# Optimization experiments

Measured on AMD Instinct MI355X. Metric: run time of the kernel, lower is better.

## Reference

```python
import jax, jax.numpy as jnp
import numpy as np

RADIUS = 50.0
EPS = 1e-8


def setup_inputs() -> dict:
    key = jax.random.key(0)
    k1, k2, k3, k4, k5 = jax.random.split(key, 5)
    N, E, H = 16384, 524288, 256
    x = jax.random.normal(k1, (N, H), dtype=jnp.float32)
    edge_index = jax.random.randint(k2, (2, E), 0, N, dtype=jnp.int32)
    spatial_coords = jax.random.uniform(k3, (N, 2), dtype=jnp.float32) * 1000.0
    w1 = jax.random.normal(k4, (3, H // 2), dtype=jnp.float32) * 0.02
    b1 = jnp.zeros((H // 2,), dtype=jnp.float32)
    w2 = jax.random.normal(k5, (H // 2, H), dtype=jnp.float32) * 0.02
    b2 = jnp.zeros((H,), dtype=jnp.float32)
    return {"x": x, "edge_index": edge_index, "spatial_coords": spatial_coords,
            "w1": w1, "b1": b1, "w2": w2, "b2": b2}


def reference(x, edge_index, spatial_coords, w1, b1, w2, b2):
    N = x.shape[0]
    row, col = edge_index[0], edge_index[1]

    # degree via scatter-add (segment_sum)
    ones = jnp.ones(row.shape, dtype=x.dtype)
    degree = jax.ops.segment_sum(ones, row, num_segments=N)  # [N]

    # spatial density: count neighbors within RADIUS (full pairwise, vectorized)
    sq = jnp.sum(spatial_coords * spatial_coords, axis=-1)  # [N]
    d2 = sq[:, None] + sq[None, :] - 2.0 * (spatial_coords @ spatial_coords.T)  # [N,N] squared dists
    in_radius = (d2 <= RADIUS * RADIUS).astype(x.dtype)
    density = jnp.sum(in_radius, axis=1) - 1.0  # exclude self
    density = density / (jnp.max(density) + EPS)

    # local feature variance: || x - mean(neighbor features) ||
    nbr_sum = jax.ops.segment_sum(x[col], row, num_segments=N)  # [N,H]
    cnt = jnp.clip(degree, 1.0)[:, None]
    nbr_mean = nbr_sum / cnt
    fvar = jnp.linalg.norm(x - nbr_mean, axis=-1)  # [N]
    fvar = fvar / (jnp.max(fvar) + EPS)

    feats = jnp.stack([degree / (jnp.max(degree) + EPS), density, fvar], axis=-1)  # [N,3]
    h = jax.nn.relu(feats @ w1 + b1)
    return h @ w2 + b2  # [N, hidden_dim]
```

## Files before the change

kernel.cpp:

```cpp
#include <hip/hip_runtime.h>
#include <math.h>

#define R2 2500.0f
#define EPSF 1e-8f

constexpr int H   = 256;
constexpr int HH  = 128;
constexpr int NB  = 8;
constexpr int BSH = 11;
constexpr int RPW = 4;

__global__ void __launch_bounds__(256) k_degcell(
    const int* __restrict__ row, const int* __restrict__ col,
    int* __restrict__ deg4, const float* __restrict__ coords,
    int* __restrict__ cellcnt, int E, int EB, int N) {
    if ((int)blockIdx.x < EB) {
        int e = blockIdx.x * 256 + threadIdx.x;
        if (e < E) atomicAdd(&deg4[row[e] * NB + (col[e] >> BSH)], 1);
    } else {
        int t = ((int)blockIdx.x - EB) * 256 + threadIdx.x;
        if (t < N) {
            float2 c = ((const float2*)coords)[t];
            int cx = (int)(c.x * 0.02f); if (cx > 19) cx = 19;
            int cy = (int)(c.y * 0.02f); if (cy > 19) cy = 19;
            atomicAdd(&cellcnt[cy * 20 + cx], 1);
        }
    }
}

__global__ void __launch_bounds__(256) k_bsum(const int* __restrict__ deg4,
                                              int* __restrict__ bsum) {
    int t = threadIdx.x;
    int4 v = ((const int4*)deg4)[blockIdx.x * 256 + t];
    int sum = v.x + v.y + v.z + v.w;
#pragma unroll
    for (int off = 32; off > 0; off >>= 1) sum += __shfl_xor(sum, off, 64);
    __shared__ int sw[4];
    if ((t & 63) == 0) sw[t >> 6] = sum;
    __syncthreads();
    if (t == 0) bsum[blockIdx.x] = sw[0] + sw[1] + sw[2] + sw[3];
}

__global__ void __launch_bounds__(512) k_scatcell(
    const int* __restrict__ deg4, const int* __restrict__ bsum,
    int* __restrict__ rp4, int* __restrict__ cur4, int M,
    const int* __restrict__ cellcnt, int* __restrict__ cellstart,
    int* __restrict__ cellcur) {
    __shared__ int s[512];
    int t = threadIdx.x;
    int blk = blockIdx.x;
    if (blk < gridDim.x - 1) {
        s[t] = (t < 128) ? bsum[t] : 0;
        __syncthreads();
        for (int off = 1; off < 128; off <<= 1) {
            int v = (t < 128) ? s[t] : 0;
            int add = (t >= off && t < 128) ? s[t - off] : 0;
            __syncthreads();
            if (t < 128) s[t] = v + add;
            __syncthreads();
        }
        int boff = (blk > 0) ? s[blk - 1] : 0;
        if (t < 256) {
            int lane = t & 63, w = t >> 6;
            int4 v = ((const int4*)deg4)[blk * 256 + t];
            int tsum = v.x + v.y + v.z + v.w;
            int incl = tsum;
#pragma unroll
            for (int off = 1; off < 64; off <<= 1) {
                int n = __shfl_up(incl, off, 64);
                if (lane >= off) incl += n;
            }
            __shared__ int wsum[4];
            if (lane == 63) wsum[w] = incl;
            __syncthreads();
            int woff = 0;
#pragma unroll
            for (int k = 0; k < 4; k++) woff += (k < w) ? wsum[k] : 0;
            int excl = boff + woff + (incl - tsum);
            int4 r;
            r.x = excl;
            r.y = excl + v.x;
            r.z = excl + v.x + v.y;
            r.w = excl + v.x + v.y + v.z;
            ((int4*)rp4)[blk * 256 + t]  = r;
            ((int4*)cur4)[blk * 256 + t] = r;
            if (blk == 127 && t == 255) rp4[M] = excl + tsum;
        }
    } else {
        s[t] = (t < 400) ? cellcnt[t] : 0;
        __syncthreads();
        for (int off = 1; off < 512; off <<= 1) {
            int v = s[t];
            int add = (t >= off) ? s[t - off] : 0;
            __syncthreads();
            s[t] = v + add;
            __syncthreads();
        }
        if (t < 400) {
            int excl = (t > 0) ? s[t - 1] : 0;
            cellstart[t] = excl;
            cellcur[t]   = excl;
        }
        if (t == 400) cellstart[400] = s[399];
    }
}

__global__ void __launch_bounds__(256) k_fillcell(
    const int* __restrict__ row, const int* __restrict__ col,
    int* __restrict__ cur4, int* __restrict__ cols,
    const float* __restrict__ coords, int* __restrict__ cellcur,
    float4* __restrict__ pts, int E, int EB, int N) {
    if ((int)blockIdx.x < EB) {
        int e = blockIdx.x * 256 + threadIdx.x;
        if (e < E) {
            int r = row[e], c = col[e];
            int p = atomicAdd(&cur4[r * NB + (c >> BSH)], 1);
            cols[p] = c;
        }
    } else {
        int t = ((int)blockIdx.x - EB) * 256 + threadIdx.x;
        if (t < N) {
            float2 c = ((const float2*)coords)[t];
            int cx = (int)(c.x * 0.02f); if (cx > 19) cx = 19;
            int cy = (int)(c.y * 0.02f); if (cy > 19) cy = 19;
            int p = atomicAdd(&cellcur[cy * 20 + cx], 1);
            pts[p] = make_float4(c.x, c.y, c.x * c.x + c.y * c.y, __int_as_float(t));
        }
    }
}

__global__ void __launch_bounds__(256) k_dgrid(
    const float4* __restrict__ pts, const int* __restrict__ cellstart,
    int* __restrict__ dens, int N) {
    int wave = threadIdx.x >> 6;
    int lane = threadIdx.x & 63;
    int t = blockIdx.x * 4 + wave;
    float4 p = pts[t];
    int cx = (int)(p.x * 0.02f); if (cx > 19) cx = 19;
    int cy = (int)(p.y * 0.02f); if (cy > 19) cy = 19;
    int x0 = cx - 2; if (x0 < 0) x0 = 0;
    int x1 = cx + 2; if (x1 > 19) x1 = 19;
    int y0 = cy - 2; if (y0 < 0) y0 = 0;
    int y1 = cy + 2; if (y1 > 19) y1 = 19;
    int cnt = 0;
    for (int yy = y0; yy <= y1; yy++) {
        int rowb = yy * 20;
        int s = cellstart[rowb + x0];
        int e = cellstart[rowb + x1 + 1];
        for (int q = s + lane; q < e; q += 64) {
            float4 pq = pts[q];
            float dot = p.x * pq.x + p.y * pq.y;
            float d2 = (p.z + pq.z) - 2.0f * dot;
            cnt += (d2 <= R2) ? 1 : 0;
        }
    }
#pragma unroll
    for (int off = 32; off > 0; off >>= 1) cnt += __shfl_xor(cnt, off, 64);
    if (lane == 0) dens[__float_as_int(p.w)] = cnt;
}

__global__ void __launch_bounds__(256) k_fvar(
    const float* __restrict__ x, const int* __restrict__ rp4,
    const int* __restrict__ cols, float* __restrict__ fvar, int N) {
    __shared__ float4 lds[4][8][64];
    int wave = threadIdx.x >> 6;
    int lane = threadIdx.x & 63;
    int i0 = (blockIdx.x * 4 + wave) * RPW;
    const float4* xb = (const float4*)x;

    int bnd = rp4[i0 * NB + (lane < 32 ? lane : 32)];

    float4 acc0 = make_float4(0.f, 0.f, 0.f, 0.f);
    float4 acc1 = make_float4(0.f, 0.f, 0.f, 0.f);
    float4 acc2 = make_float4(0.f, 0.f, 0.f, 0.f);
    float4 acc3 = make_float4(0.f, 0.f, 0.f, 0.f);

    for (int b = 0; b < NB; b++) {
        int s0 = __shfl(bnd, b, 64),      e0 = __shfl(bnd, b + 1, 64);
        int s1 = __shfl(bnd, 8 + b, 64),  e1 = __shfl(bnd, 9 + b, 64);
        int s2 = __shfl(bnd, 16 + b, 64), e2 = __shfl(bnd, 17 + b, 64);
        int s3 = __shfl(bnd, 24 + b, 64), e3 = __shfl(bnd, 25 + b, 64);
        int m0 = e0 - s0, m1 = e1 - s1, m2 = e2 - s2;
        int c1 = m0, c2 = m0 + m1, c3 = m0 + m1 + m2;
        int mt = c3 + (e3 - s3);
        if (mt == 0) continue;

        int j = lane;
        int rowj = (j >= c1) + (j >= c2) + (j >= c3);
        int base = (rowj == 0) ? s0 : (rowj == 1) ? (s1 - c1)
                 : (rowj == 2) ? (s2 - c2) : (s3 - c3);
        int pos = base + j;
        if (j >= mt) pos = s0;
        int colj = cols[pos];

        int mtc = (mt > 64) ? 64 : mt;
        for (int j0 = 0; j0 < mtc; j0 += 8) {
            int nb2 = mtc - j0; if (nb2 > 8) nb2 = 8;
#pragma unroll
            for (int k = 0; k < 8; k++) {
                if (k < nb2) {
                    int c = __shfl(colj, j0 + k, 64);
                    const float4* gp = xb + (size_t)c * 64 + lane;
                    __builtin_amdgcn_global_load_lds(
                        (const __attribute__((address_space(1))) void*)gp,
                        (__attribute__((address_space(3))) void*)(&lds[wave][k][0]),
                        16, 0, 0);
                }
            }
            __builtin_amdgcn_s_waitcnt(0);
#pragma unroll
            for (int k = 0; k < 8; k++) {
                if (k < nb2) {
                    int rk = __shfl(rowj, j0 + k, 64);
                    float4 v = lds[wave][k][lane];
                    float w0 = (rk == 0) ? 1.0f : 0.0f;
                    float w1 = (rk == 1) ? 1.0f : 0.0f;
                    float w2 = (rk == 2) ? 1.0f : 0.0f;
                    float w3 = (rk == 3) ? 1.0f : 0.0f;
                    acc0.x = fmaf(v.x, w0, acc0.x); acc0.y = fmaf(v.y, w0, acc0.y);
                    acc0.z = fmaf(v.z, w0, acc0.z); acc0.w = fmaf(v.w, w0, acc0.w);
                    acc1.x = fmaf(v.x, w1, acc1.x); acc1.y = fmaf(v.y, w1, acc1.y);
                    acc1.z = fmaf(v.z, w1, acc1.z); acc1.w = fmaf(v.w, w1, acc1.w);
                    acc2.x = fmaf(v.x, w2, acc2.x); acc2.y = fmaf(v.y, w2, acc2.y);
                    acc2.z = fmaf(v.z, w2, acc2.z); acc2.w = fmaf(v.w, w2, acc2.w);
                    acc3.x = fmaf(v.x, w3, acc3.x); acc3.y = fmaf(v.y, w3, acc3.y);
                    acc3.z = fmaf(v.z, w3, acc3.z); acc3.w = fmaf(v.w, w3, acc3.w);
                }
            }
        }
        if (mt > 64) {
            for (int jq = 64; jq < mt; jq++) {
                int rk = (jq >= c1) + (jq >= c2) + (jq >= c3);
                int pq = ((rk == 0) ? s0 : (rk == 1) ? (s1 - c1)
                        : (rk == 2) ? (s2 - c2) : (s3 - c3)) + jq;
                float4 v = xb[(size_t)cols[pq] * 64 + lane];
                float w0 = (rk == 0) ? 1.0f : 0.0f;
                float w1 = (rk == 1) ? 1.0f : 0.0f;
                float w2 = (rk == 2) ? 1.0f : 0.0f;
                float w3 = (rk == 3) ? 1.0f : 0.0f;
                acc0.x = fmaf(v.x, w0, acc0.x); acc0.y = fmaf(v.y, w0, acc0.y);
                acc0.z = fmaf(v.z, w0, acc0.z); acc0.w = fmaf(v.w, w0, acc0.w);
                acc1.x = fmaf(v.x, w1, acc1.x); acc1.y = fmaf(v.y, w1, acc1.y);
                acc1.z = fmaf(v.z, w1, acc1.z); acc1.w = fmaf(v.w, w1, acc1.w);
                acc2.x = fmaf(v.x, w2, acc2.x); acc2.y = fmaf(v.y, w2, acc2.y);
                acc2.z = fmaf(v.z, w2, acc2.z); acc2.w = fmaf(v.w, w2, acc2.w);
                acc3.x = fmaf(v.x, w3, acc3.x); acc3.y = fmaf(v.y, w3, acc3.y);
                acc3.z = fmaf(v.z, w3, acc3.z); acc3.w = fmaf(v.w, w3, acc3.w);
            }
        }
    }

#define FIN(RR, ACCR)                                                   \
    {                                                                   \
        int i = i0 + (RR);                                              \
        float cnt = fmaxf((float)(__shfl(bnd, (RR) * NB + NB, 64) -     \
                                  __shfl(bnd, (RR) * NB, 64)), 1.0f);   \
        float4 xi = xb[(size_t)i * 64 + lane];                          \
        float dx = xi.x - ACCR.x / cnt;                                 \
        float dy = xi.y - ACCR.y / cnt;                                 \
        float dz = xi.z - ACCR.z / cnt;                                 \
        float dw = xi.w - ACCR.w / cnt;                                 \
        float ss = dx * dx + dy * dy + dz * dz + dw * dw;               \
        _Pragma("unroll")                                               \
        for (int off = 32; off > 0; off >>= 1) ss += __shfl_xor(ss, off, 64); \
        if (lane == 0) fvar[i] = sqrtf(ss);                             \
    }

    FIN(0, acc0);
    FIN(1, acc1);
    FIN(2, acc2);
    FIN(3, acc3);
#undef FIN
}

__global__ void __launch_bounds__(256) k_scal(
    const int* __restrict__ rp4, const int* __restrict__ dens,
    const float* __restrict__ fvar, int* __restrict__ scal, int N) {
    __shared__ int sd[4], sn[4];
    __shared__ float sf[4];
    int t = threadIdx.x;
    int g = blockIdx.x * 256 + t;
    int stride = 256 * gridDim.x;
    int md = 0, mn = 0;
    float mf = 0.f;
    for (int i = g; i < N; i += stride) {
        md = max(md, rp4[(i + 1) * NB] - rp4[i * NB]);
        mn = max(mn, dens[i]);
        mf = fmaxf(mf, fvar[i]);
    }
#pragma unroll
    for (int off = 32; off > 0; off >>= 1) {
        md = max(md, __shfl_xor(md, off, 64));
        mn = max(mn, __shfl_xor(mn, off, 64));
        mf = fmaxf(mf, __shfl_xor(mf, off, 64));
    }
    int w = t >> 6, l = t & 63;
    if (l == 0) { sd[w] = md; sn[w] = mn; sf[w] = mf; }
    __syncthreads();
    if (t == 0) {
#pragma unroll
        for (int k = 1; k < 4; k++) {
            md = max(md, sd[k]);
            mn = max(mn, sn[k]);
            mf = fmaxf(mf, sf[k]);
        }
        atomicMax(&scal[0], md);
        atomicMax(&scal[1], mn);
        atomicMax(&scal[2], __float_as_int(mf));
    }
}

__global__ void __launch_bounds__(256) k_mlp(
    const float* __restrict__ w1, const float* __restrict__ b1,
    const float* __restrict__ w2, const float* __restrict__ b2,
    const int* __restrict__ rp4, const int* __restrict__ dens,
    const float* __restrict__ fvar, const int* __restrict__ scal,
    float* __restrict__ out, int N) {
    __shared__ float sh_h[HH];
    int j = threadIdx.x;
    float wv[HH];
#pragma unroll
    for (int l = 0; l < HH; l++) wv[l] = w2[l * H + j];
    float bj = b2[j];
    float maxdeg  = (float)scal[0] + EPSF;
    float maxdens = (float)(scal[1] - 1) + EPSF;
    float maxfv   = __int_as_float(scal[2]) + EPSF;
    float w1a = 0.f, w1b = 0.f, w1c = 0.f, b1j = 0.f;
    if (j < HH) { w1a = w1[j]; w1b = w1[HH + j]; w1c = w1[2 * HH + j]; b1j = b1[j]; }
    for (int i = blockIdx.x; i < N; i += gridDim.x) {
        float f0 = (float)(rp4[(i + 1) * NB] - rp4[i * NB]) / maxdeg;
        float f1 = (float)(dens[i] - 1) / maxdens;
        float f2 = fvar[i] / maxfv;
        if (j < HH) {
            float h = f0 * w1a + f1 * w1b + f2 * w1c + b1j;
            sh_h[j] = fmaxf(h, 0.0f);
        }
        __syncthreads();
        float acc = bj;
#pragma unroll
        for (int l = 0; l < HH; l++) acc = fmaf(sh_h[l], wv[l], acc);
        out[(size_t)i * H + j] = acc;
        __syncthreads();
    }
}

extern "C" void kernel_launch(void* const* d_in, const int* in_sizes, int n_in,
                              void* d_out, int out_size, void* d_ws, size_t ws_size,
                              hipStream_t stream) {
    const float* x      = (const float*)d_in[0];
    const int*   ei     = (const int*)d_in[1];
    const float* coords = (const float*)d_in[2];
    const float* w1     = (const float*)d_in[3];
    const float* b1     = (const float*)d_in[4];
    const float* w2     = (const float*)d_in[5];
    const float* b2     = (const float*)d_in[6];
    float* out = (float*)d_out;

    const int N = in_sizes[2] / 2;
    const int E = in_sizes[1] / 2;
    const int M = N * NB;
    const int NBLK = M / 1024;
    const int EB = (E + 255) / 256;
    const int CB = N / 256;
    const int* row = ei;
    const int* col = ei + E;

    int* ws        = (int*)d_ws;
    int* scal      = ws;
    int* deg4      = ws + 4;
    int* cellcnt   = ws + 4 + M;
    int* rp4       = ws + 408 + M;
    int* cur4      = rp4 + M + 4;
    int* cellstart = cur4 + M;
    int* cellcur   = cellstart + 404;
    int* dens_cnt  = cellcur + 400;
    float* fvarp   = (float*)(dens_cnt + N);
    int* bsum      = dens_cnt + 2 * N;
    int* boff      = bsum + 128;
    int* cols      = boff + 128;
    float4* pts    = (float4*)(cols + E);

    hipMemsetAsync(ws, 0, (size_t)(408 + M) * sizeof(int), stream);

    k_degcell<<<EB + CB, 256, 0, stream>>>(row, col, deg4, coords, cellcnt, E, EB, N);
    k_bsum<<<NBLK, 256, 0, stream>>>(deg4, bsum);
    k_scatcell<<<NBLK + 1, 512, 0, stream>>>(deg4, bsum, rp4, cur4, M,
                                             cellcnt, cellstart, cellcur);
    k_fillcell<<<EB + CB, 256, 0, stream>>>(row, col, cur4, cols,
                                            coords, cellcur, pts, E, EB, N);

    k_dgrid<<<N / 4, 256, 0, stream>>>(pts, cellstart, dens_cnt, N);

    k_fvar<<<N / (4 * RPW), 256, 0, stream>>>(x, rp4, cols, fvarp, N);

    k_scal<<<64, 256, 0, stream>>>(rp4, dens_cnt, fvarp, scal, N);

    k_mlp<<<1024, 256, 0, stream>>>(w1, b1, w2, b2, rp4, dens_cnt, fvarp, scal,
                                    out, N);
}
```

Measured before the change: 255.6 us.

## Replace LDS-staged neighbor gather with per-row register gathers in fvar kernel

```diff
diff --git a/kernel.cpp b/kernel.cpp
--- a/kernel.cpp
+++ b/kernel.cpp
@@ -159,10 +159,9 @@
     if (lane == 0) dens[__float_as_int(p.w)] = cnt;
 }
 
-__global__ void __launch_bounds__(256) k_fvar(
+__global__ void __launch_bounds__(256, 4) k_fvar(
     const float* __restrict__ x, const int* __restrict__ rp4,
     const int* __restrict__ cols, float* __restrict__ fvar, int N) {
-    __shared__ float4 lds[4][8][64];
     int wave = threadIdx.x >> 6;
     int lane = threadIdx.x & 63;
     int i0 = (blockIdx.x * 4 + wave) * RPW;
@@ -176,76 +175,49 @@
     float4 acc3 = make_float4(0.f, 0.f, 0.f, 0.f);
 
     for (int b = 0; b < NB; b++) {
-        int s0 = __shfl(bnd, b, 64),      e0 = __shfl(bnd, b + 1, 64);
-        int s1 = __shfl(bnd, 8 + b, 64),  e1 = __shfl(bnd, 9 + b, 64);
-        int s2 = __shfl(bnd, 16 + b, 64), e2 = __shfl(bnd, 17 + b, 64);
-        int s3 = __shfl(bnd, 24 + b, 64), e3 = __shfl(bnd, 25 + b, 64);
-        int m0 = e0 - s0, m1 = e1 - s1, m2 = e2 - s2;
-        int c1 = m0, c2 = m0 + m1, c3 = m0 + m1 + m2;
-        int mt = c3 + (e3 - s3);
-        if (mt == 0) continue;
-
-        int j = lane;
-        int rowj = (j >= c1) + (j >= c2) + (j >= c3);
-        int base = (rowj == 0) ? s0 : (rowj == 1) ? (s1 - c1)
-                 : (rowj == 2) ? (s2 - c2) : (s3 - c3);
-        int pos = base + j;
-        if (j >= mt) pos = s0;
-        int colj = cols[pos];
-
-        int mtc = (mt > 64) ? 64 : mt;
-        for (int j0 = 0; j0 < mtc; j0 += 8) {
-            int nb2 = mtc - j0; if (nb2 > 8) nb2 = 8;
-#pragma unroll
-            for (int k = 0; k < 8; k++) {
-                if (k < nb2) {
-                    int c = __shfl(colj, j0 + k, 64);
-                    const float4* gp = xb + (size_t)c * 64 + lane;
-                    __builtin_amdgcn_global_load_lds(
-                        (const __attribute__((address_space(1))) void*)gp,
-                        (__attribute__((address_space(3))) void*)(&lds[wave][k][0]),
-                        16, 0, 0);
+#pragma unroll
+        for (int r = 0; r < RPW; r++) {
+            float4& a = (r == 0) ? acc0 : (r == 1) ? acc1 : (r == 2) ? acc2 : acc3;
+            int s = __shfl(bnd, r * NB + b, 64);
+            int e = __shfl(bnd, r * NB + b + 1, 64);
+            for (int p0 = s; p0 < e; p0 += 64) {
+                int m = e - p0; if (m > 64) m = 64;
+                int idx = cols[p0 + (lane < m ? lane : m - 1)];
+                for (int j = 0; j < m; j += 8) {
+                    int nb2 = m - j; if (nb2 > 8) nb2 = 8;
+                    float4 g0 = xb[(size_t)__shfl(idx, j + 0, 64) * 64 + lane];
+                    float4 g1 = xb[(size_t)__shfl(idx, j + 1, 64) * 64 + lane];
+                    float4 g2 = xb[(size_t)__shfl(idx, j + 2, 64) * 64 + lane];
+                    float4 g3 = xb[(size_t)__shfl(idx, j + 3, 64) * 64 + lane];
+                    float4 g4 = xb[(size_t)__shfl(idx, j + 4, 64) * 64 + lane];
+                    float4 g5 = xb[(size_t)__shfl(idx, j + 5, 64) * 64 + lane];
+                    float4 g6 = xb[(size_t)__shfl(idx, j + 6, 64) * 64 + lane];
+                    float4 g7 = xb[(size_t)__shfl(idx, j + 7, 64) * 64 + lane];
+                    float w0 = (1 < nb2 + 1) ? 1.0f : 0.0f;
+                    float w1 = (1 < nb2) ? 1.0f : 0.0f;
+                    float w2 = (2 < nb2) ? 1.0f : 0.0f;
+                    float w3 = (3 < nb2) ? 1.0f : 0.0f;
+                    float w4 = (4 < nb2) ? 1.0f : 0.0f;
+                    float w5 = (5 < nb2) ? 1.0f : 0.0f;
+                    float w6 = (6 < nb2) ? 1.0f : 0.0f;
+                    float w7 = (7 < nb2) ? 1.0f : 0.0f;
+                    a.x = fmaf(g0.x, w0, a.x); a.y = fmaf(g0.y, w0, a.y);
+                    a.z = fmaf(g0.z, w0, a.z); a.w = fmaf(g0.w, w0, a.w);
+                    a.x = fmaf(g1.x, w1, a.x); a.y = fmaf(g1.y, w1, a.y);
+                    a.z = fmaf(g1.z, w1, a.z); a.w = fmaf(g1.w, w1, a.w);
+                    a.x = fmaf(g2.x, w2, a.x); a.y = fmaf(g2.y, w2, a.y);
+                    a.z = fmaf(g2.z, w2, a.z); a.w = fmaf(g2.w, w2, a.w);
+                    a.x = fmaf(g3.x, w3, a.x); a.y = fmaf(g3.y, w3, a.y);
+                    a.z = fmaf(g3.z, w3, a.z); a.w = fmaf(g3.w, w3, a.w);
+                    a.x = fmaf(g4.x, w4, a.x); a.y = fmaf(g4.y, w4, a.y);
+                    a.z = fmaf(g4.z, w4, a.z); a.w = fmaf(g4.w, w4, a.w);
+                    a.x = fmaf(g5.x, w5, a.x); a.y = fmaf(g5.y, w5, a.y);
+                    a.z = fmaf(g5.z, w5, a.z); a.w = fmaf(g5.w, w5, a.w);
+                    a.x = fmaf(g6.x, w6, a.x); a.y = fmaf(g6.y, w6, a.y);
+                    a.z = fmaf(g6.z, w6, a.z); a.w = fmaf(g6.w, w6, a.w);
+                    a.x = fmaf(g7.x, w7, a.x); a.y = fmaf(g7.y, w7, a.y);
+                    a.z = fmaf(g7.z, w7, a.z); a.w = fmaf(g7.w, w7, a.w);
                 }
-            }
-            __builtin_amdgcn_s_waitcnt(0);
-#pragma unroll
-            for (int k = 0; k < 8; k++) {
-                if (k < nb2) {
-                    int rk = __shfl(rowj, j0 + k, 64);
-                    float4 v = lds[wave][k][lane];
-                    float w0 = (rk == 0) ? 1.0f : 0.0f;
-                    float w1 = (rk == 1) ? 1.0f : 0.0f;
-                    float w2 = (rk == 2) ? 1.0f : 0.0f;
-                    float w3 = (rk == 3) ? 1.0f : 0.0f;
-                    acc0.x = fmaf(v.x, w0, acc0.x); acc0.y = fmaf(v.y, w0, acc0.y);
-                    acc0.z = fmaf(v.z, w0, acc0.z); acc0.w = fmaf(v.w, w0, acc0.w);
-                    acc1.x = fmaf(v.x, w1, acc1.x); acc1.y = fmaf(v.y, w1, acc1.y);
-                    acc1.z = fmaf(v.z, w1, acc1.z); acc1.w = fmaf(v.w, w1, acc1.w);
-                    acc2.x = fmaf(v.x, w2, acc2.x); acc2.y = fmaf(v.y, w2, acc2.y);
-                    acc2.z = fmaf(v.z, w2, acc2.z); acc2.w = fmaf(v.w, w2, acc2.w);
-                    acc3.x = fmaf(v.x, w3, acc3.x); acc3.y = fmaf(v.y, w3, acc3.y);
-                    acc3.z = fmaf(v.z, w3, acc3.z); acc3.w = fmaf(v.w, w3, acc3.w);
-                }
-            }
-        }
-        if (mt > 64) {
-            for (int jq = 64; jq < mt; jq++) {
-                int rk = (jq >= c1) + (jq >= c2) + (jq >= c3);
-                int pq = ((rk == 0) ? s0 : (rk == 1) ? (s1 - c1)
-                        : (rk == 2) ? (s2 - c2) : (s3 - c3)) + jq;
-                float4 v = xb[(size_t)cols[pq] * 64 + lane];
-                float w0 = (rk == 0) ? 1.0f : 0.0f;
-                float w1 = (rk == 1) ? 1.0f : 0.0f;
-                float w2 = (rk == 2) ? 1.0f : 0.0f;
-                float w3 = (rk == 3) ? 1.0f : 0.0f;
-                acc0.x = fmaf(v.x, w0, acc0.x); acc0.y = fmaf(v.y, w0, acc0.y);
-                acc0.z = fmaf(v.z, w0, acc0.z); acc0.w = fmaf(v.w, w0, acc0.w);
-                acc1.x = fmaf(v.x, w1, acc1.x); acc1.y = fmaf(v.y, w1, acc1.y);
-                acc1.z = fmaf(v.z, w1, acc1.z); acc1.w = fmaf(v.w, w1, acc1.w);
-                acc2.x = fmaf(v.x, w2, acc2.x); acc2.y = fmaf(v.y, w2, acc2.y);
-                acc2.z = fmaf(v.z, w2, acc2.z); acc2.w = fmaf(v.w, w2, acc2.w);
-                acc3.x = fmaf(v.x, w3, acc3.x); acc3.y = fmaf(v.y, w3, acc3.y);
-                acc3.z = fmaf(v.z, w3, acc3.z); acc3.w = fmaf(v.w, w3, acc3.w);
             }
         }
     }
```

New measurement: 246.6 us. 1.04x faster.
